# Kernel tuning notes

Hardware: AMD Instinct MI355X
Metric: run time of the kernel (lower is better)

Reference implementation:

```python
import jax, jax.numpy as jnp
import numpy as np

N = 100_000      # atom_count
E = 6_400_000    # number of (directed) edges, avg degree 64
BOX = 100.0      # simulation box edge length


def setup_inputs() -> dict:
    key = jax.random.key(0)
    k1, k2, k3 = jax.random.split(key, 3)
    pos = jax.random.uniform(k1, (N, 3), dtype=jnp.float32) * BOX
    src = jax.random.randint(k2, (E,), 0, N, dtype=jnp.int32)
    # offset in [1, N) guarantees dst != src (no zero-distance self edges)
    off = jax.random.randint(k3, (E,), 1, N, dtype=jnp.int32)
    dst = ((src + off) % N).astype(jnp.int32)
    edge_index = jnp.stack([src, dst], axis=0)  # [2, E]
    sigma = jnp.asarray(0.3, dtype=jnp.float32)
    epsilon = jnp.asarray(1.0, dtype=jnp.float32)
    return {"pos": pos, "sigma": sigma, "epsilon": epsilon, "edge_index": edge_index}


def _total_energy(pos, sigma, epsilon, src, dst):
    # r = edge_attr: per-edge distance, differentiable w.r.t. pos
    d = pos[src] - pos[dst]                      # [E, 3] gather + subtract
    r = jnp.sqrt(jnp.sum(d * d, axis=-1))        # [E]
    sr6 = (sigma / r) ** 6
    # potential_formula: 4*epsilon*((sigma/r)**12 - (sigma/r)**6)
    v_r = 4.0 * epsilon * (sr6 * sr6 - sr6)      # [E]
    return v_r.sum()


def reference(pos, sigma, epsilon, edge_index):
    src, dst = edge_index[0], edge_index[1]
    energy = _total_energy(pos, sigma, epsilon, src, dst)
    # afc: autograd force — grad of summed pair potential w.r.t. positions
    # (per-edge force scattered onto atoms by edge_index; grad does the
    #  gather-compute-scatter in one pass)
    pair_force = jax.grad(_total_energy, argnums=0)(pos, sigma, epsilon, src, dst)
    atom_force = -pair_force / 2.0               # /2: each pair counted twice
    return energy, atom_force
```

## Files before the change

kernel.cpp:

```cpp
#include <hip/hip_runtime.h>


#define NBINS      8
#define BIN_ATOMS  12800
#define BIN_F      (BIN_ATOMS * 3)
#define ROW_F      (NBINS * BIN_F)
#define BLOCK      1024
#define MAXCHUNKS  32

__global__ __launch_bounds__(BLOCK, 1) void pairforce_binned(
    const float* __restrict__ pos,
    const float* __restrict__ sigma_p,
    const float* __restrict__ eps_p,
    const int*   __restrict__ src,
    const int*   __restrict__ dst,
    float* __restrict__ frep,
    float* __restrict__ erep,
    int nEdges, int chunkEdges)
{
    extern __shared__ float sh[];
    const int t = threadIdx.x;
    const int b = blockIdx.x % NBINS;
    const int c = blockIdx.x / NBINS;

    for (int j = t; j < (BIN_F + 16) / 4; j += BLOCK)
        ((float4*)sh)[j] = make_float4(0.f, 0.f, 0.f, 0.f);
    __syncthreads();

    const float sigma = sigma_p[0];
    const float eps   = eps_p[0];
    const float sig2  = sigma * sigma;
    const int binStart = b * BIN_ATOMS;

    const int start = c * chunkEdges;
    const int end   = min(start + chunkEdges, nEdges);

    const int4* src4 = (const int4*)src;
    const int4* dst4 = (const int4*)dst;

    float ev = 0.0f;

    for (int i4 = (start >> 2) + t; i4 < (end >> 2); i4 += BLOCK) {
        const int4 s4 = src4[i4];
        const int4 d4 = dst4[i4];
        #pragma unroll
        for (int k = 0; k < 4; ++k) {
            const int s = (k == 0) ? s4.x : (k == 1) ? s4.y : (k == 2) ? s4.z : s4.w;
            const int d = (k == 0) ? d4.x : (k == 1) ? d4.y : (k == 2) ? d4.z : d4.w;
            const unsigned ls = (unsigned)(s - binStart);
            const unsigned ld = (unsigned)(d - binStart);
            const bool hs = ls < BIN_ATOMS;
            const bool hd = ld < BIN_ATOMS;
            if (hs | hd) {
                const float dx = pos[3 * s + 0] - pos[3 * d + 0];
                const float dy = pos[3 * s + 1] - pos[3 * d + 1];
                const float dz = pos[3 * s + 2] - pos[3 * d + 2];
                const float r2     = dx * dx + dy * dy + dz * dz;
                const float inv_r2 = 1.0f / r2;
                const float s2     = sig2 * inv_r2;
                const float sr6    = s2 * s2 * s2;
                const float sr12   = sr6 * sr6;
                const float fs = 12.0f * eps * (2.0f * sr12 - sr6) * inv_r2;
                const float fx = fs * dx;
                const float fy = fs * dy;
                const float fz = fs * dz;
                if (hs) {
                    atomicAdd(&sh[3 * ls + 0],  fx);
                    atomicAdd(&sh[3 * ls + 1],  fy);
                    atomicAdd(&sh[3 * ls + 2],  fz);
                    ev += 4.0f * eps * (sr12 - sr6);
                }
                if (hd) {
                    atomicAdd(&sh[3 * ld + 0], -fx);
                    atomicAdd(&sh[3 * ld + 1], -fy);
                    atomicAdd(&sh[3 * ld + 2], -fz);
                }
            }
        }
    }

    #pragma unroll
    for (int off = 32; off > 0; off >>= 1)
        ev += __shfl_down(ev, off, 64);
    if ((t & 63) == 0) sh[BIN_F + (t >> 6)] = ev;
    __syncthreads();

    float4* outSeg = (float4*)(frep + (size_t)c * ROW_F + (size_t)b * BIN_F);
    for (int j = t; j < BIN_F / 4; j += BLOCK)
        outSeg[j] = ((float4*)sh)[j];

    if (t == 0) {
        float e = 0.f;
        #pragma unroll
        for (int w = 0; w < 16; ++w) e += sh[BIN_F + w];
        erep[blockIdx.x] = e;
    }
}

__global__ __launch_bounds__(256) void pairforce_reduce(
    const float* __restrict__ frep,
    const float* __restrict__ erep,
    float* __restrict__ out,
    int n3, int nChunks, int nPart)
{
    const int i = blockIdx.x * 256 + threadIdx.x;
    if (i < n3) {
        float acc = 0.f;
        for (int c = 0; c < nChunks; ++c)
            acc += frep[(size_t)c * ROW_F + i];
        out[1 + i] = acc;
    }
    if (blockIdx.x == gridDim.x - 1) {
        float e = 0.f;
        for (int j = threadIdx.x; j < nPart; j += 256) e += erep[j];
        #pragma unroll
        for (int off = 32; off > 0; off >>= 1) e += __shfl_down(e, off, 64);
        __shared__ float ep[4];
        if ((threadIdx.x & 63) == 0) ep[threadIdx.x >> 6] = e;
        __syncthreads();
        if (threadIdx.x == 0) out[0] = ep[0] + ep[1] + ep[2] + ep[3];
    }
}

extern "C" void kernel_launch(void* const* d_in, const int* in_sizes, int n_in,
                              void* d_out, int out_size, void* d_ws, size_t ws_size,
                              hipStream_t stream)
{
    const float* pos     = (const float*)d_in[0];
    const float* sigma_p = (const float*)d_in[1];
    const float* eps_p   = (const float*)d_in[2];
    const int*   edge    = (const int*)d_in[3];

    const int nEdges = in_sizes[3] / 2;
    const int* src = edge;
    const int* dst = edge + nEdges;

    const int n3 = out_size - 1;

    const size_t rowBytes = (size_t)ROW_F * sizeof(float);
    int nChunks = (int)((ws_size - 4096) / rowBytes);
    if (nChunks > MAXCHUNKS) nChunks = MAXCHUNKS;
    if (nChunks < 1) nChunks = 1;

    const int chunkEdges = (((nEdges + nChunks - 1) / nChunks) + 3) & ~3;

    float* frep = (float*)d_ws;
    float* erep = frep + (size_t)nChunks * ROW_F;

    const size_t shbytes = (size_t)(BIN_F + 16) * sizeof(float);

    const int grid1 = nChunks * NBINS;
    pairforce_binned<<<grid1, BLOCK, shbytes, stream>>>(
        pos, sigma_p, eps_p, src, dst, frep, erep, nEdges, chunkEdges);

    const int grid2 = (n3 + 255) / 256;
    pairforce_reduce<<<grid2, 256, 0, stream>>>(
        frep, erep, (float*)d_out, n3, nChunks, nChunks * NBINS);
}
```

Before: 313.1 us.

## Pre-bucket edges by atom bin before shared-memory force accumulation

Adds a scatter pass that writes each directed edge as two compact records into per-wave, per-bin buckets, and pads positions to float4. The accumulation kernel then processes only the records for its bin, with positions staged in LDS. This replaces the old scheme in which every bin block rescanned the full edge list, cutting redundant global index reads. The trade-off is extra bucket write and read traffic, fixed bucket capacities that could silently drop edges if a bin overflows, and dependence on the atom count fitting the bin layout.

```diff
diff --git a/kernel.cpp b/kernel.cpp
--- a/kernel.cpp
+++ b/kernel.cpp
@@ -1,12 +1,177 @@
 #include <hip/hip_runtime.h>
 
+
+#define ROW_F   307200
+
+#define NB2     16
+#define BA2     6400
+#define BF2     (BA2 * 3)
+#define KCH     16
+#define SCG     256
+#define SCB     512
+#define NWAVES  2048
+#define CAP     512
 
 #define NBINS      8
 #define BIN_ATOMS  12800
 #define BIN_F      (BIN_ATOMS * 3)
-#define ROW_F      (NBINS * BIN_F)
 #define BLOCK      1024
 #define MAXCHUNKS  32
+
+__global__ __launch_bounds__(SCB) void pf_scatter(
+    const float* __restrict__ pos,
+    float4*      __restrict__ pos4,
+    const int*   __restrict__ src,
+    const int*   __restrict__ dst,
+    unsigned*    __restrict__ buckets,
+    unsigned*    __restrict__ cnt,
+    int nEdges, int nAtoms)
+{
+    __shared__ unsigned shcur[(SCB / 64) * NB2];
+    const int t = threadIdx.x, lane = t & 63, wv = t >> 6;
+    if (t < (SCB / 64) * NB2) shcur[t] = 0;
+
+    for (int i = blockIdx.x * SCB + t; i < nAtoms; i += SCG * SCB)
+        pos4[i] = make_float4(pos[3 * i + 0], pos[3 * i + 1], pos[3 * i + 2], 0.f);
+
+    __syncthreads();
+
+    unsigned* mycur = shcur + wv * NB2;
+    const int w    = blockIdx.x * (SCB / 64) + wv;
+    const int epw  = (nEdges + NWAVES - 1) / NWAVES;
+    const int ebeg = w * epw;
+    const int eend = min(nEdges, ebeg + epw);
+
+    int  e   = ebeg + lane;
+    bool act = e < eend;
+    int  s = 0, d = 0;
+    if (act) { s = src[e]; d = dst[e]; }
+
+    for (int base = ebeg; base < eend; base += 64) {
+        const int  en   = base + 64 + lane;
+        const bool actn = en < eend;
+        int sn = 0, dn = 0;
+        if (actn) { sn = src[en]; dn = dst[en]; }
+        if (act) {
+            const unsigned su = (unsigned)s, du = (unsigned)d;
+            const unsigned sb = su / BA2, db = du / BA2;
+            const unsigned recS = ((su - sb * BA2) << 18) | (1u << 17) | du;
+            const unsigned recD = ((du - db * BA2) << 18) | su;
+            const unsigned is = atomicAdd(&mycur[sb], 1u);
+            if (is < CAP) buckets[((size_t)w * NB2 + sb) * CAP + is] = recS;
+            const unsigned id = atomicAdd(&mycur[db], 1u);
+            if (id < CAP) buckets[((size_t)w * NB2 + db) * CAP + id] = recD;
+        }
+        act = actn; s = sn; d = dn;
+    }
+    __syncthreads();
+    if (lane < NB2) {
+        const unsigned cv = mycur[lane];
+        cnt[w * NB2 + lane] = cv < CAP ? cv : CAP;
+    }
+}
+
+__global__ __launch_bounds__(1024, 1) void pf_accum(
+    const float*    __restrict__ pos,
+    const float4*   __restrict__ pos4,
+    const float*    __restrict__ sigma_p,
+    const float*    __restrict__ eps_p,
+    const unsigned* __restrict__ buckets,
+    const unsigned* __restrict__ cnt,
+    float* __restrict__ frep,
+    float* __restrict__ erep,
+    int nAtoms)
+{
+    extern __shared__ float sh[];
+    float* shp = sh + BF2 + 16;
+    const int t = threadIdx.x, lane = t & 63, v = t >> 6;
+    const int b = blockIdx.x / KCH;
+    const int c = blockIdx.x % KCH;
+
+    for (int j = t; j < (BF2 + 16) / 4; j += 1024)
+        ((float4*)sh)[j] = make_float4(0.f, 0.f, 0.f, 0.f);
+
+    const int binStart = b * BA2;
+    const int binCnt   = min(BA2, nAtoms - binStart);
+    const int nf       = binCnt * 3;
+    const float4* gp   = (const float4*)(pos + (size_t)binStart * 3);
+    for (int j = t; j < (nf >> 2); j += 1024) ((float4*)shp)[j] = gp[j];
+    for (int j = (nf & ~3) + t; j < nf; j += 1024) shp[j] = pos[binStart * 3 + j];
+    __syncthreads();
+
+    const float sigma = sigma_p[0], eps = eps_p[0];
+    const float sig2 = sigma * sigma;
+    const float c12 = 12.f * eps, c4 = 4.f * eps;
+
+    float ev = 0.f;
+    const int slot = c * 16 + v;
+    for (int k = 0; k < NWAVES / 256; ++k) {
+        const int w = slot + (k << 8);
+        const int n = cnt[w * NB2 + b];
+        const unsigned* seg = buckets + ((size_t)w * NB2 + b) * CAP;
+        for (int j = lane; j < n; j += 64) {
+            const unsigned rec = seg[j];
+            const int   la = rec >> 18;
+            const int   o  = rec & 0x1FFFF;
+            const float fl = (rec & (1u << 17)) ? 1.f : 0.f;
+            const float ax = shp[3 * la + 0];
+            const float ay = shp[3 * la + 1];
+            const float az = shp[3 * la + 2];
+            const float4 po = pos4[o];
+            const float dx = ax - po.x, dy = ay - po.y, dz = az - po.z;
+            const float r2   = dx * dx + dy * dy + dz * dz;
+            const float ir2  = 1.0f / r2;
+            const float s2   = sig2 * ir2;
+            const float sr6  = s2 * s2 * s2;
+            const float sr12 = sr6 * sr6;
+            const float fs   = c12 * (2.f * sr12 - sr6) * ir2;
+            atomicAdd(&sh[3 * la + 0], fs * dx);
+            atomicAdd(&sh[3 * la + 1], fs * dy);
+            atomicAdd(&sh[3 * la + 2], fs * dz);
+            ev += fl * c4 * (sr12 - sr6);
+        }
+    }
+
+    #pragma unroll
+    for (int off = 32; off > 0; off >>= 1) ev += __shfl_down(ev, off, 64);
+    if (lane == 0) sh[BF2 + v] = ev;
+    __syncthreads();
+
+    float4* outSeg = (float4*)(frep + (size_t)c * ROW_F + (size_t)b * BF2);
+    for (int j = t; j < BF2 / 4; j += 1024) outSeg[j] = ((float4*)sh)[j];
+
+    if (t == 0) {
+        float e = 0.f;
+        #pragma unroll
+        for (int w2 = 0; w2 < 16; ++w2) e += sh[BF2 + w2];
+        erep[blockIdx.x] = e;
+    }
+}
+
+__global__ __launch_bounds__(256) void pairforce_reduce(
+    const float* __restrict__ frep,
+    const float* __restrict__ erep,
+    float* __restrict__ out,
+    int n3, int nChunks, int nPart)
+{
+    const int i = blockIdx.x * 256 + threadIdx.x;
+    if (i < n3) {
+        float acc = 0.f;
+        for (int c = 0; c < nChunks; ++c)
+            acc += frep[(size_t)c * ROW_F + i];
+        out[1 + i] = acc;
+    }
+    if (blockIdx.x == gridDim.x - 1) {
+        float e = 0.f;
+        for (int j = threadIdx.x; j < nPart; j += 256) e += erep[j];
+        #pragma unroll
+        for (int off = 32; off > 0; off >>= 1) e += __shfl_down(e, off, 64);
+        __shared__ float ep[4];
+        if ((threadIdx.x & 63) == 0) ep[threadIdx.x >> 6] = e;
+        __syncthreads();
+        if (threadIdx.x == 0) out[0] = ep[0] + ep[1] + ep[2] + ep[3];
+    }
+}
 
 __global__ __launch_bounds__(BLOCK, 1) void pairforce_binned(
     const float* __restrict__ pos,
@@ -97,31 +262,6 @@
     }
 }
 
-__global__ __launch_bounds__(256) void pairforce_reduce(
-    const float* __restrict__ frep,
-    const float* __restrict__ erep,
-    float* __restrict__ out,
-    int n3, int nChunks, int nPart)
-{
-    const int i = blockIdx.x * 256 + threadIdx.x;
-    if (i < n3) {
-        float acc = 0.f;
-        for (int c = 0; c < nChunks; ++c)
-            acc += frep[(size_t)c * ROW_F + i];
-        out[1 + i] = acc;
-    }
-    if (blockIdx.x == gridDim.x - 1) {
-        float e = 0.f;
-        for (int j = threadIdx.x; j < nPart; j += 256) e += erep[j];
-        #pragma unroll
-        for (int off = 32; off > 0; off >>= 1) e += __shfl_down(e, off, 64);
-        __shared__ float ep[4];
-        if ((threadIdx.x & 63) == 0) ep[threadIdx.x >> 6] = e;
-        __syncthreads();
-        if (threadIdx.x == 0) out[0] = ep[0] + ep[1] + ep[2] + ep[3];
-    }
-}
-
 extern "C" void kernel_launch(void* const* d_in, const int* in_sizes, int n_in,
                               void* d_out, int out_size, void* d_ws, size_t ws_size,
                               hipStream_t stream)
@@ -136,6 +276,26 @@
     const int* dst = edge + nEdges;
 
     const int n3 = out_size - 1;
+    const int nAtoms = n3 / 3;
+
+    size_t off = 0;
+    float*    pos4    = (float*)d_ws;                    off += (size_t)(NB2 * BA2) * 16;
+    unsigned* buckets = (unsigned*)((char*)d_ws + off);  off += (size_t)NWAVES * NB2 * CAP * 4;
+    unsigned* cntp    = (unsigned*)((char*)d_ws + off);  off += (size_t)NWAVES * NB2 * 4;
+    float*    frepN   = (float*)((char*)d_ws + off);     off += (size_t)KCH * ROW_F * 4;
+    float*    erepN   = (float*)((char*)d_ws + off);     off += 256 * 4;
+
+    if (ws_size >= off && nAtoms <= NB2 * BA2) {
+        pf_scatter<<<SCG, SCB, 0, stream>>>(pos, (float4*)pos4, src, dst,
+                                            buckets, cntp, nEdges, nAtoms);
+        const size_t shb = (size_t)(BF2 + 16 + BF2) * sizeof(float);
+        pf_accum<<<NB2 * KCH, 1024, shb, stream>>>(pos, (const float4*)pos4,
+                                                   sigma_p, eps_p, buckets, cntp,
+                                                   frepN, erepN, nAtoms);
+        pairforce_reduce<<<(n3 + 255) / 256, 256, 0, stream>>>(
+            frepN, erepN, (float*)d_out, n3, KCH, NB2 * KCH);
+        return;
+    }
 
     const size_t rowBytes = (size_t)ROW_F * sizeof(float);
     int nChunks = (int)((ws_size - 4096) / rowBytes);
```

Result: slower. 373.2 us (+19.2%).

## Bucket edges into atom-bin pair tiles and compute each edge once

Applied to the files above, without the earlier changes.

Adds a counting-sort pipeline: edges are counted and placed into per-tile buckets indexed by (min bin, max bin) pair across 32 atom bins. Each tile block then stages both bins' positions in LDS and computes each edge exactly once, accumulating forces for both endpoints in LDS. This replaces the old scheme, where each of 8 bins rescanned every edge and gathered positions from global memory. The cost is three extra preprocessing kernels that read the edge list twice and write a packed record array, plus per-tile load imbalance.

```diff
diff --git a/kernel.cpp b/kernel.cpp
--- a/kernel.cpp
+++ b/kernel.cpp
@@ -1,12 +1,252 @@
 #include <hip/hip_runtime.h>
 
+
+#define NBIN   32
+#define BA     3200
+#define BF     (BA * 3)
+#define NT     528
+#define SEGS   512
+#define ROW_F  307200
 
 #define NBINS      8
 #define BIN_ATOMS  12800
 #define BIN_F      (BIN_ATOMS * 3)
-#define ROW_F      (NBINS * BIN_F)
 #define BLOCK      1024
 #define MAXCHUNKS  32
+
+typedef __attribute__((ext_vector_type(4))) int ivec4;
+
+__device__ __forceinline__ ivec4 nt_load_i4(const int* p) {
+    return __builtin_nontemporal_load((const ivec4*)p);
+}
+__device__ __forceinline__ void lds_fadd(float* p, float v) {
+    __hip_atomic_fetch_add(p, v, __ATOMIC_RELAXED, __HIP_MEMORY_SCOPE_WORKGROUP);
+}
+__device__ __forceinline__ unsigned lds_uinc(unsigned* p) {
+    return __hip_atomic_fetch_add(p, 1u, __ATOMIC_RELAXED, __HIP_MEMORY_SCOPE_WORKGROUP);
+}
+
+__device__ __forceinline__ unsigned tile_of(unsigned bs, unsigned bd) {
+    const unsigned i = min(bs, bd), j = max(bs, bd);
+    return ((i * (2u * NBIN + 1u - i)) >> 1) + (j - i);
+}
+
+__global__ __launch_bounds__(1024) void pf_count(
+    const int* __restrict__ src, const int* __restrict__ dst,
+    unsigned* __restrict__ cnt, int nEdges)
+{
+    __shared__ unsigned c[NT];
+    const int t = threadIdx.x;
+    const int bid = (int)blockIdx.x;
+    if (t < NT) c[t] = 0;
+    __syncthreads();
+
+    const int eblk  = ((nEdges + SEGS - 1) / SEGS + 3) & ~3;
+    const int ebeg  = bid * eblk;
+    const int eend  = (ebeg + eblk < nEdges) ? (ebeg + eblk) : nEdges;
+    const int i4beg = ebeg >> 2;
+    const int i4end = eend >> 2;
+
+    for (int i4 = i4beg + t; i4 < i4end; i4 += 1024) {
+        const ivec4 s4 = nt_load_i4(src + 4 * i4);
+        const ivec4 d4 = nt_load_i4(dst + 4 * i4);
+        #pragma unroll
+        for (int k = 0; k < 4; ++k) {
+            const unsigned bs = (unsigned)s4[k] / BA;
+            const unsigned bd = (unsigned)d4[k] / BA;
+            lds_uinc(&c[tile_of(bs, bd)]);
+        }
+    }
+    __syncthreads();
+    if (t < NT) cnt[bid * NT + t] = c[t];
+}
+
+__global__ __launch_bounds__(1024) void pf_prefix(
+    const unsigned* __restrict__ cnt, unsigned* __restrict__ base,
+    unsigned* __restrict__ tileStart)
+{
+    __shared__ unsigned colTot[NT], ts[NT + 1];
+    const int t = threadIdx.x;
+    if (t < NT) {
+        unsigned run = 0;
+        for (int s = 0; s < SEGS; ++s) {
+            base[s * NT + t] = run;
+            run += cnt[s * NT + t];
+        }
+        colTot[t] = run;
+    }
+    __syncthreads();
+    if (t == 0) {
+        unsigned run = 0;
+        for (int k = 0; k < NT; ++k) { ts[k] = run; run += colTot[k]; }
+        ts[NT] = run;
+    }
+    __syncthreads();
+    if (t < NT) {
+        const unsigned add = ts[t];
+        for (int s = 0; s < SEGS; ++s) base[s * NT + t] += add;
+    }
+    if (t <= NT) tileStart[t] = ts[t];
+}
+
+__global__ __launch_bounds__(1024) void pf_place(
+    const int* __restrict__ src, const int* __restrict__ dst,
+    const unsigned* __restrict__ base, unsigned* __restrict__ recs, int nEdges)
+{
+    __shared__ unsigned cur[NT];
+    const int t = threadIdx.x;
+    const int bid = (int)blockIdx.x;
+    if (t < NT) cur[t] = base[bid * NT + t];
+    __syncthreads();
+
+    const int eblk  = ((nEdges + SEGS - 1) / SEGS + 3) & ~3;
+    const int ebeg  = bid * eblk;
+    const int eend  = (ebeg + eblk < nEdges) ? (ebeg + eblk) : nEdges;
+    const int i4beg = ebeg >> 2;
+    const int i4end = eend >> 2;
+
+    for (int i4 = i4beg + t; i4 < i4end; i4 += 1024) {
+        const ivec4 s4 = nt_load_i4(src + 4 * i4);
+        const ivec4 d4 = nt_load_i4(dst + 4 * i4);
+        #pragma unroll
+        for (int k = 0; k < 4; ++k) {
+            const unsigned su = (unsigned)s4[k], du = (unsigned)d4[k];
+            const unsigned bs = su / BA, bd = du / BA;
+            unsigned a = su, b = du;
+            if (bd < bs) { a = du; b = su; }
+            const unsigned i = min(bs, bd), j = max(bs, bd);
+            const unsigned li = a - i * BA, lj = b - j * BA;
+            const unsigned tl = ((i * (2u * NBIN + 1u - i)) >> 1) + (j - i);
+            const unsigned idx = lds_uinc(&cur[tl]);
+            recs[idx] = (li << 12) | lj;
+        }
+    }
+}
+
+__global__ __launch_bounds__(1024) void pf_accum2(
+    const float* __restrict__ pos,
+    const float* __restrict__ sigma_p, const float* __restrict__ eps_p,
+    const unsigned* __restrict__ recs, const unsigned* __restrict__ tileStart,
+    float* __restrict__ frep,
+    float* __restrict__ erep,
+    int nAtoms)
+{
+    extern __shared__ float sh[];
+    const int t = threadIdx.x, lane = t & 63, v = t >> 6;
+
+    int i = 0, rem = (int)blockIdx.x;
+    while (rem >= NBIN - i) { rem -= NBIN - i; ++i; }
+    const int j = i + rem;
+    const bool diag = (i == j);
+
+    float* sPosI = sh;
+    float* sPosJ = diag ? sh : sh + BF;
+    float* sFI   = sh + 2 * BF;
+    float* sFJ   = diag ? sFI : sh + 3 * BF;
+    float* sE    = sh + 4 * BF;
+
+    for (int k = t; k < (2 * BF + 16) / 4; k += 1024)
+        ((float4*)(sh + 2 * BF))[k] = make_float4(0.f, 0.f, 0.f, 0.f);
+
+    {
+        const int aI = i * BA;
+        int nf = nAtoms - aI; if (nf > BA) nf = BA; if (nf < 0) nf = 0; nf *= 3;
+        const float* g = pos + (size_t)aI * 3;
+        for (int k = t; k < (nf >> 2); k += 1024) ((float4*)sPosI)[k] = ((const float4*)g)[k];
+        for (int k = (nf & ~3) + t; k < nf; k += 1024) sPosI[k] = g[k];
+    }
+    if (!diag) {
+        const int aJ = j * BA;
+        int nf = nAtoms - aJ; if (nf > BA) nf = BA; if (nf < 0) nf = 0; nf *= 3;
+        const float* g = pos + (size_t)aJ * 3;
+        for (int k = t; k < (nf >> 2); k += 1024) ((float4*)sPosJ)[k] = ((const float4*)g)[k];
+        for (int k = (nf & ~3) + t; k < nf; k += 1024) sPosJ[k] = g[k];
+    }
+    __syncthreads();
+
+    const float sigma = sigma_p[0], eps = eps_p[0];
+    const float sig2 = sigma * sigma;
+    const float c12 = 12.f * eps, c4 = 4.f * eps;
+
+    const int rBeg = (int)tileStart[blockIdx.x];
+    const int rEnd = (int)tileStart[blockIdx.x + 1];
+    float ev = 0.f;
+
+    for (int r0 = rBeg; r0 < rEnd; r0 += 4 * 1024) {
+        unsigned rc[4]; bool ac[4];
+        #pragma unroll
+        for (int k = 0; k < 4; ++k) {
+            const int idx = r0 + k * 1024 + t;
+            ac[k] = idx < rEnd;
+            rc[k] = ac[k] ? recs[idx] : 0u;
+        }
+        #pragma unroll
+        for (int k = 0; k < 4; ++k) {
+            const int li = rc[k] >> 12, lj = rc[k] & 0xFFF;
+            const float ax = sPosI[3 * li + 0], ay = sPosI[3 * li + 1], az = sPosI[3 * li + 2];
+            const float bx = sPosJ[3 * lj + 0], by = sPosJ[3 * lj + 1], bz = sPosJ[3 * lj + 2];
+            const float dx = ax - bx, dy = ay - by, dz = az - bz;
+            const float r2   = dx * dx + dy * dy + dz * dz;
+            const float ir2  = 1.0f / r2;
+            const float s2   = sig2 * ir2;
+            const float sr6  = s2 * s2 * s2;
+            const float sr12 = sr6 * sr6;
+            const float fs   = c12 * (2.f * sr12 - sr6) * ir2;
+            if (ac[k]) {
+                lds_fadd(&sFI[3 * li + 0],  fs * dx);
+                lds_fadd(&sFI[3 * li + 1],  fs * dy);
+                lds_fadd(&sFI[3 * li + 2],  fs * dz);
+                lds_fadd(&sFJ[3 * lj + 0], -fs * dx);
+                lds_fadd(&sFJ[3 * lj + 1], -fs * dy);
+                lds_fadd(&sFJ[3 * lj + 2], -fs * dz);
+                ev += c4 * (sr12 - sr6);
+            }
+        }
+    }
+
+    #pragma unroll
+    for (int off = 32; off > 0; off >>= 1) ev += __shfl_down(ev, off, 64);
+    if (lane == 0) sE[v] = ev;
+    __syncthreads();
+
+    float4* dI = (float4*)(frep + (size_t)j * ROW_F + (size_t)i * BF);
+    for (int k = t; k < BF / 4; k += 1024) dI[k] = ((float4*)sFI)[k];
+    if (!diag) {
+        float4* dJ = (float4*)(frep + (size_t)i * ROW_F + (size_t)j * BF);
+        for (int k = t; k < BF / 4; k += 1024) dJ[k] = ((float4*)sFJ)[k];
+    }
+    if (t == 0) {
+        float e = 0.f;
+        #pragma unroll
+        for (int w = 0; w < 16; ++w) e += sE[w];
+        erep[blockIdx.x] = e;
+    }
+}
+
+__global__ __launch_bounds__(256) void pairforce_reduce(
+    const float* __restrict__ frep,
+    const float* __restrict__ erep,
+    float* __restrict__ out,
+    int n3, int nChunks, int nPart)
+{
+    const int i = blockIdx.x * 256 + threadIdx.x;
+    if (i < n3) {
+        float acc = 0.f;
+        for (int c = 0; c < nChunks; ++c)
+            acc += frep[(size_t)c * ROW_F + i];
+        out[1 + i] = acc;
+    }
+    if (blockIdx.x == gridDim.x - 1) {
+        float e = 0.f;
+        for (int jj = threadIdx.x; jj < nPart; jj += 256) e += erep[jj];
+        #pragma unroll
+        for (int off = 32; off > 0; off >>= 1) e += __shfl_down(e, off, 64);
+        __shared__ float ep[4];
+        if ((threadIdx.x & 63) == 0) ep[threadIdx.x >> 6] = e;
+        __syncthreads();
+        if (threadIdx.x == 0) out[0] = ep[0] + ep[1] + ep[2] + ep[3];
+    }
+}
 
 __global__ __launch_bounds__(BLOCK, 1) void pairforce_binned(
     const float* __restrict__ pos,
@@ -23,8 +263,8 @@
     const int b = blockIdx.x % NBINS;
     const int c = blockIdx.x / NBINS;
 
-    for (int j = t; j < (BIN_F + 16) / 4; j += BLOCK)
-        ((float4*)sh)[j] = make_float4(0.f, 0.f, 0.f, 0.f);
+    for (int jj = t; jj < (BIN_F + 16) / 4; jj += BLOCK)
+        ((float4*)sh)[jj] = make_float4(0.f, 0.f, 0.f, 0.f);
     __syncthreads();
 
     const float sigma = sigma_p[0];
@@ -86,39 +326,14 @@
     __syncthreads();
 
     float4* outSeg = (float4*)(frep + (size_t)c * ROW_F + (size_t)b * BIN_F);
-    for (int j = t; j < BIN_F / 4; j += BLOCK)
-        outSeg[j] = ((float4*)sh)[j];
+    for (int jj = t; jj < BIN_F / 4; jj += BLOCK)
+        outSeg[jj] = ((float4*)sh)[jj];
 
     if (t == 0) {
         float e = 0.f;
         #pragma unroll
         for (int w = 0; w < 16; ++w) e += sh[BIN_F + w];
         erep[blockIdx.x] = e;
-    }
-}
-
-__global__ __launch_bounds__(256) void pairforce_reduce(
-    const float* __restrict__ frep,
-    const float* __restrict__ erep,
-    float* __restrict__ out,
-    int n3, int nChunks, int nPart)
-{
-    const int i = blockIdx.x * 256 + threadIdx.x;
-    if (i < n3) {
-        float acc = 0.f;
-        for (int c = 0; c < nChunks; ++c)
-            acc += frep[(size_t)c * ROW_F + i];
-        out[1 + i] = acc;
-    }
-    if (blockIdx.x == gridDim.x - 1) {
-        float e = 0.f;
-        for (int j = threadIdx.x; j < nPart; j += 256) e += erep[j];
-        #pragma unroll
-        for (int off = 32; off > 0; off >>= 1) e += __shfl_down(e, off, 64);
-        __shared__ float ep[4];
-        if ((threadIdx.x & 63) == 0) ep[threadIdx.x >> 6] = e;
-        __syncthreads();
-        if (threadIdx.x == 0) out[0] = ep[0] + ep[1] + ep[2] + ep[3];
     }
 }
 
@@ -136,6 +351,28 @@
     const int* dst = edge + nEdges;
 
     const int n3 = out_size - 1;
+    const int nAtoms = n3 / 3;
+
+    auto alignup = [](size_t x) { return (x + 255) & ~(size_t)255; };
+    size_t off = 0;
+    unsigned* recs   = (unsigned*)((char*)d_ws + off); off = alignup(off + (size_t)nEdges * 4);
+    unsigned* cntp   = (unsigned*)((char*)d_ws + off); off = alignup(off + (size_t)SEGS * NT * 4);
+    unsigned* basep  = (unsigned*)((char*)d_ws + off); off = alignup(off + (size_t)SEGS * NT * 4);
+    unsigned* tstart = (unsigned*)((char*)d_ws + off); off = alignup(off + (size_t)(NT + 1) * 4);
+    float*    frepN  = (float*)((char*)d_ws + off);    off = alignup(off + (size_t)NBIN * ROW_F * 4);
+    float*    erepN  = (float*)((char*)d_ws + off);    off = alignup(off + (size_t)NT * 4);
+
+    if (ws_size >= off && nAtoms <= NBIN * BA && nEdges > 0 && (nEdges & 3) == 0) {
+        pf_count<<<SEGS, 1024, 0, stream>>>(src, dst, cntp, nEdges);
+        pf_prefix<<<1, 1024, 0, stream>>>(cntp, basep, tstart);
+        pf_place<<<SEGS, 1024, 0, stream>>>(src, dst, basep, recs, nEdges);
+        const size_t shb = (size_t)(4 * BF + 16) * sizeof(float);
+        pf_accum2<<<NT, 1024, shb, stream>>>(pos, sigma_p, eps_p, recs, tstart,
+                                             frepN, erepN, nAtoms);
+        pairforce_reduce<<<(n3 + 255) / 256, 256, 0, stream>>>(
+            frepN, erepN, (float*)d_out, n3, NBIN, NT);
+        return;
+    }
 
     const size_t rowBytes = (size_t)ROW_F * sizeof(float);
     int nChunks = (int)((ws_size - 4096) / rowBytes);
```

Result: slower. 559.1 us (+78.6%).

## Bucket edges by atom bin via counting sort before force accumulation

Applied to the files above, without the earlier changes.

Replaces the chunk×bin scan, in which every block reads all edges of its chunk, with a counting-sort pipeline. Edges are histogrammed into segment/bin/column buckets, prefix-scanned, and written out as packed per-endpoint records. The accumulate kernel then reads only the records for its own bin and keeps that bin's positions in LDS. This removes the redundant edge reads across bins, at the cost of several extra kernel launches and a full pass writing and reading 2E records. It falls back to the old path when the workspace or input shape does not fit.

```diff
diff --git a/kernel.cpp b/kernel.cpp
--- a/kernel.cpp
+++ b/kernel.cpp
@@ -1,12 +1,267 @@
 #include <hip/hip_runtime.h>
 
+
+#define NBIN   32
+#define BA     3200
+#define BF     (BA * 3)
+#define SEGS   256
+#define NCOL   64
+#define BPS    (NBIN * NCOL)
+#define NBUCK  (SEGS * BPS)
+#define NROW   16
+#define ROW_F  307200
 
 #define NBINS      8
 #define BIN_ATOMS  12800
 #define BIN_F      (BIN_ATOMS * 3)
-#define ROW_F      (NBINS * BIN_F)
 #define BLOCK      1024
 #define MAXCHUNKS  32
+
+typedef __attribute__((ext_vector_type(4))) int ivec4;
+
+__device__ __forceinline__ ivec4 nt_load_i4(const int* p) {
+    return __builtin_nontemporal_load((const ivec4*)p);
+}
+__device__ __forceinline__ void lds_fadd(float* p, float v) {
+    __hip_atomic_fetch_add(p, v, __ATOMIC_RELAXED, __HIP_MEMORY_SCOPE_WORKGROUP);
+}
+__device__ __forceinline__ unsigned lds_uinc(unsigned* p) {
+    return __hip_atomic_fetch_add(p, 1u, __ATOMIC_RELAXED, __HIP_MEMORY_SCOPE_WORKGROUP);
+}
+
+__global__ __launch_bounds__(1024) void pf_count(
+    const float* __restrict__ pos, float4* __restrict__ pos4,
+    const int* __restrict__ src, const int* __restrict__ dst,
+    unsigned* __restrict__ cnt, int nEdges, int nAtoms)
+{
+    __shared__ unsigned h[BPS];
+    const int t = threadIdx.x, bid = (int)blockIdx.x;
+    h[t] = 0; h[t + 1024] = 0;
+
+    for (int i = bid * 1024 + t; i < nAtoms; i += SEGS * 1024)
+        pos4[i] = make_float4(pos[3 * i + 0], pos[3 * i + 1], pos[3 * i + 2], 0.f);
+    __syncthreads();
+
+    const int eblk  = ((nEdges + SEGS - 1) / SEGS + 3) & ~3;
+    const int ebeg  = bid * eblk;
+    const int eend  = (ebeg + eblk < nEdges) ? (ebeg + eblk) : nEdges;
+    for (int i4 = (ebeg >> 2) + t; i4 < (eend >> 2); i4 += 1024) {
+        const ivec4 s4 = nt_load_i4(src + 4 * i4);
+        const ivec4 d4 = nt_load_i4(dst + 4 * i4);
+        #pragma unroll
+        for (int k = 0; k < 4; ++k) {
+            const unsigned su = (unsigned)s4[k], du = (unsigned)d4[k];
+            lds_uinc(&h[(su / BA) * NCOL + (su & 63u)]);
+            lds_uinc(&h[(du / BA) * NCOL + (du & 63u)]);
+        }
+    }
+    __syncthreads();
+    cnt[bid * BPS + t] = h[t];
+    cnt[bid * BPS + 1024 + t] = h[t + 1024];
+}
+
+__global__ __launch_bounds__(1024) void pf_scanA(
+    const unsigned* __restrict__ cnt, unsigned* __restrict__ bstart,
+    unsigned* __restrict__ btot)
+{
+    __shared__ unsigned wt[16], wo[16];
+    const int t = threadIdx.x, lane = t & 63, wv = t >> 6;
+    const int gid = (int)blockIdx.x * 1024 + t;
+    const unsigned v = cnt[gid];
+    unsigned x = v;
+    #pragma unroll
+    for (int off = 1; off < 64; off <<= 1) {
+        const unsigned n = __shfl_up(x, off, 64);
+        if (lane >= off) x += n;
+    }
+    if (lane == 63) wt[wv] = x;
+    __syncthreads();
+    if (t == 0) {
+        unsigned run = 0;
+        #pragma unroll
+        for (int w = 0; w < 16; ++w) { wo[w] = run; run += wt[w]; }
+        btot[blockIdx.x] = run;
+    }
+    __syncthreads();
+    bstart[gid] = (x - v) + wo[wv];
+}
+
+__global__ __launch_bounds__(512) void pf_scanB(
+    const unsigned* __restrict__ btot, unsigned* __restrict__ boffs)
+{
+    __shared__ unsigned wt[8], wo[8];
+    const int t = threadIdx.x, lane = t & 63, wv = t >> 6;
+    const unsigned v = btot[t];
+    unsigned x = v;
+    #pragma unroll
+    for (int off = 1; off < 64; off <<= 1) {
+        const unsigned n = __shfl_up(x, off, 64);
+        if (lane >= off) x += n;
+    }
+    if (lane == 63) wt[wv] = x;
+    __syncthreads();
+    if (t == 0) {
+        unsigned run = 0;
+        #pragma unroll
+        for (int w = 0; w < 8; ++w) { wo[w] = run; run += wt[w]; }
+    }
+    __syncthreads();
+    boffs[t] = (x - v) + wo[wv];
+}
+
+__global__ __launch_bounds__(1024) void pf_scanC(
+    unsigned* __restrict__ bstart, const unsigned* __restrict__ boffs, int nRec)
+{
+    const int gid = (int)blockIdx.x * 1024 + threadIdx.x;
+    bstart[gid] += boffs[blockIdx.x];
+    if (gid == 0) bstart[NBUCK] = (unsigned)nRec;
+}
+
+__global__ __launch_bounds__(1024) void pf_place(
+    const int* __restrict__ src, const int* __restrict__ dst,
+    const unsigned* __restrict__ bstart, unsigned* __restrict__ recs, int nEdges)
+{
+    __shared__ unsigned cur[BPS];
+    const int t = threadIdx.x, bid = (int)blockIdx.x;
+    cur[t] = bstart[bid * BPS + t];
+    cur[t + 1024] = bstart[bid * BPS + 1024 + t];
+    __syncthreads();
+
+    const int eblk  = ((nEdges + SEGS - 1) / SEGS + 3) & ~3;
+    const int ebeg  = bid * eblk;
+    const int eend  = (ebeg + eblk < nEdges) ? (ebeg + eblk) : nEdges;
+    for (int i4 = (ebeg >> 2) + t; i4 < (eend >> 2); i4 += 1024) {
+        const ivec4 s4 = nt_load_i4(src + 4 * i4);
+        const ivec4 d4 = nt_load_i4(dst + 4 * i4);
+        #pragma unroll
+        for (int k = 0; k < 4; ++k) {
+            const unsigned su = (unsigned)s4[k], du = (unsigned)d4[k];
+            const unsigned ob_s = su / BA, ob_d = du / BA;
+            const unsigned is = lds_uinc(&cur[ob_s * NCOL + (su & 63u)]);
+            recs[is] = ((su - ob_s * BA) << 18) | (1u << 17) | du;
+            const unsigned id = lds_uinc(&cur[ob_d * NCOL + (du & 63u)]);
+            recs[id] = ((du - ob_d * BA) << 18) | su;
+        }
+    }
+}
+
+__global__ __launch_bounds__(512) void pf_accum3(
+    const float* __restrict__ pos, const float4* __restrict__ pos4,
+    const float* __restrict__ sigma_p, const float* __restrict__ eps_p,
+    const unsigned* __restrict__ recs, const unsigned* __restrict__ bstart,
+    float* __restrict__ frep,
+    float* __restrict__ erep,
+    int nAtoms)
+{
+    extern __shared__ float sh[];
+    float* sF = sh;
+    float* sE = sh + BF;
+    float* sP = sh + BF + 8;
+    const int t = threadIdx.x, lane = t & 63, wv = t >> 6;
+    const int obin = (int)blockIdx.x >> 4;
+    const int SC   = (int)blockIdx.x & 15;
+
+    for (int k = t; k < (BF + 8) / 4; k += 512)
+        ((float4*)sF)[k] = make_float4(0.f, 0.f, 0.f, 0.f);
+    {
+        const int aS = obin * BA;
+        int nf = nAtoms - aS; if (nf > BA) nf = BA; if (nf < 0) nf = 0; nf *= 3;
+        const float* g = pos + (size_t)aS * 3;
+        for (int k = t; k < (nf >> 2); k += 512) ((float4*)sP)[k] = ((const float4*)g)[k];
+        for (int k = (nf & ~3) + t; k < nf; k += 512) sP[k] = g[k];
+    }
+    __syncthreads();
+
+    const float sigma = sigma_p[0], eps = eps_p[0];
+    const float sig2 = sigma * sigma;
+    const float c12 = 12.f * eps, c4 = 4.f * eps;
+
+    float ev = 0.f;
+    #pragma unroll
+    for (int q = 0; q < 2; ++q) {
+        const int seg = SC * 16 + (t >> 6) + q * 8;
+        const int bkt = seg * BPS + obin * NCOL + (t & 63);
+        const int beg = (int)bstart[bkt];
+        const int end = (int)bstart[bkt + 1];
+
+        for (int r = beg; r < end; r += 2) {
+            const unsigned rec0 = recs[r];
+            const bool v1 = (r + 1) < end;
+            const unsigned rec1 = v1 ? recs[r + 1] : 0u;
+            const int l0 = rec0 >> 18, o0 = rec0 & 0x1FFFF;
+            const int l1 = rec1 >> 18, o1 = rec1 & 0x1FFFF;
+            const float4 p0 = pos4[o0];
+            const float4 p1 = pos4[o1];
+            const float a0x = sP[3 * l0 + 0], a0y = sP[3 * l0 + 1], a0z = sP[3 * l0 + 2];
+            const float a1x = sP[3 * l1 + 0], a1y = sP[3 * l1 + 1], a1z = sP[3 * l1 + 2];
+
+            const float d0x = a0x - p0.x, d0y = a0y - p0.y, d0z = a0z - p0.z;
+            const float r20  = d0x * d0x + d0y * d0y + d0z * d0z;
+            const float ir20 = 1.0f / r20;
+            const float s20  = sig2 * ir20;
+            const float sr60 = s20 * s20 * s20;
+            const float sr120 = sr60 * sr60;
+            const float fs0  = c12 * (2.f * sr120 - sr60) * ir20;
+
+            const float d1x = a1x - p1.x, d1y = a1y - p1.y, d1z = a1z - p1.z;
+            const float r21  = d1x * d1x + d1y * d1y + d1z * d1z;
+            const float ir21 = 1.0f / r21;
+            const float s21  = sig2 * ir21;
+            const float sr61 = s21 * s21 * s21;
+            const float sr121 = sr61 * sr61;
+            const float fs1  = c12 * (2.f * sr121 - sr61) * ir21;
+
+            lds_fadd(&sF[3 * l0 + 0], fs0 * d0x);
+            lds_fadd(&sF[3 * l0 + 1], fs0 * d0y);
+            lds_fadd(&sF[3 * l0 + 2], fs0 * d0z);
+            ev += (rec0 & (1u << 17)) ? c4 * (sr120 - sr60) : 0.f;
+            if (v1) {
+                lds_fadd(&sF[3 * l1 + 0], fs1 * d1x);
+                lds_fadd(&sF[3 * l1 + 1], fs1 * d1y);
+                lds_fadd(&sF[3 * l1 + 2], fs1 * d1z);
+                ev += (rec1 & (1u << 17)) ? c4 * (sr121 - sr61) : 0.f;
+            }
+        }
+    }
+
+    #pragma unroll
+    for (int off = 32; off > 0; off >>= 1) ev += __shfl_down(ev, off, 64);
+    if (lane == 0) sE[wv] = ev;
+    __syncthreads();
+
+    float4* d = (float4*)(frep + (size_t)SC * ROW_F + (size_t)obin * BF);
+    for (int k = t; k < BF / 4; k += 512) d[k] = ((const float4*)sF)[k];
+    if (t == 0) {
+        float e = 0.f;
+        #pragma unroll
+        for (int w = 0; w < 8; ++w) e += sE[w];
+        erep[blockIdx.x] = e;
+    }
+}
+
+__global__ __launch_bounds__(256) void pairforce_reduce(
+    const float* __restrict__ frep,
+    const float* __restrict__ erep,
+    float* __restrict__ out, int n3, int nChunks, int nPart)
+{
+    const int i = blockIdx.x * 256 + threadIdx.x;
+    if (i < n3) {
+        float acc = 0.f;
+        for (int c = 0; c < nChunks; ++c)
+            acc += frep[(size_t)c * ROW_F + i];
+        out[1 + i] = acc;
+    }
+    if (blockIdx.x == gridDim.x - 1) {
+        float e = 0.f;
+        for (int jj = threadIdx.x; jj < nPart; jj += 256) e += erep[jj];
+        #pragma unroll
+        for (int off = 32; off > 0; off >>= 1) e += __shfl_down(e, off, 64);
+        __shared__ float ep[4];
+        if ((threadIdx.x & 63) == 0) ep[threadIdx.x >> 6] = e;
+        __syncthreads();
+        if (threadIdx.x == 0) out[0] = ep[0] + ep[1] + ep[2] + ep[3];
+    }
+}
 
 __global__ __launch_bounds__(BLOCK, 1) void pairforce_binned(
     const float* __restrict__ pos,
@@ -23,8 +278,8 @@
     const int b = blockIdx.x % NBINS;
     const int c = blockIdx.x / NBINS;
 
-    for (int j = t; j < (BIN_F + 16) / 4; j += BLOCK)
-        ((float4*)sh)[j] = make_float4(0.f, 0.f, 0.f, 0.f);
+    for (int jj = t; jj < (BIN_F + 16) / 4; jj += BLOCK)
+        ((float4*)sh)[jj] = make_float4(0.f, 0.f, 0.f, 0.f);
     __syncthreads();
 
     const float sigma = sigma_p[0];
@@ -86,39 +341,14 @@
     __syncthreads();
 
     float4* outSeg = (float4*)(frep + (size_t)c * ROW_F + (size_t)b * BIN_F);
-    for (int j = t; j < BIN_F / 4; j += BLOCK)
-        outSeg[j] = ((float4*)sh)[j];
+    for (int jj = t; jj < BIN_F / 4; jj += BLOCK)
+        outSeg[jj] = ((float4*)sh)[jj];
 
     if (t == 0) {
         float e = 0.f;
         #pragma unroll
         for (int w = 0; w < 16; ++w) e += sh[BIN_F + w];
         erep[blockIdx.x] = e;
-    }
-}
-
-__global__ __launch_bounds__(256) void pairforce_reduce(
-    const float* __restrict__ frep,
-    const float* __restrict__ erep,
-    float* __restrict__ out,
-    int n3, int nChunks, int nPart)
-{
-    const int i = blockIdx.x * 256 + threadIdx.x;
-    if (i < n3) {
-        float acc = 0.f;
-        for (int c = 0; c < nChunks; ++c)
-            acc += frep[(size_t)c * ROW_F + i];
-        out[1 + i] = acc;
-    }
-    if (blockIdx.x == gridDim.x - 1) {
-        float e = 0.f;
-        for (int j = threadIdx.x; j < nPart; j += 256) e += erep[j];
-        #pragma unroll
-        for (int off = 32; off > 0; off >>= 1) e += __shfl_down(e, off, 64);
-        __shared__ float ep[4];
-        if ((threadIdx.x & 63) == 0) ep[threadIdx.x >> 6] = e;
-        __syncthreads();
-        if (threadIdx.x == 0) out[0] = ep[0] + ep[1] + ep[2] + ep[3];
     }
 }
 
@@ -136,6 +366,35 @@
     const int* dst = edge + nEdges;
 
     const int n3 = out_size - 1;
+    const int nAtoms = n3 / 3;
+    const int nRec = 2 * nEdges;
+
+    auto alignup = [](size_t x) { return (x + 255) & ~(size_t)255; };
+    size_t off = 0;
+    unsigned* recs   = (unsigned*)((char*)d_ws + off); off = alignup(off + (size_t)nRec * 4);
+    unsigned* cntp   = (unsigned*)((char*)d_ws + off); off = alignup(off + (size_t)NBUCK * 4);
+    unsigned* bstart = (unsigned*)((char*)d_ws + off); off = alignup(off + (size_t)(NBUCK + 1) * 4);
+    unsigned* btot   = (unsigned*)((char*)d_ws + off); off = alignup(off + 512 * 4);
+    unsigned* boffs  = (unsigned*)((char*)d_ws + off); off = alignup(off + 512 * 4);
+    float*    pos4   = (float*)((char*)d_ws + off);    off = alignup(off + (size_t)(NBIN * BA) * 16);
+    float*    frepN  = (float*)((char*)d_ws + off);    off = alignup(off + (size_t)NROW * ROW_F * 4);
+    float*    erepN  = (float*)((char*)d_ws + off);    off = alignup(off + (size_t)(NBIN * NROW) * 4);
+
+    if (ws_size >= off && nAtoms <= NBIN * BA && nEdges > 0 && (nEdges & 3) == 0) {
+        pf_count<<<SEGS, 1024, 0, stream>>>(pos, (float4*)pos4, src, dst,
+                                            cntp, nEdges, nAtoms);
+        pf_scanA<<<NBUCK / 1024, 1024, 0, stream>>>(cntp, bstart, btot);
+        pf_scanB<<<1, 512, 0, stream>>>(btot, boffs);
+        pf_scanC<<<NBUCK / 1024, 1024, 0, stream>>>(bstart, boffs, nRec);
+        pf_place<<<SEGS, 1024, 0, stream>>>(src, dst, bstart, recs, nEdges);
+        const size_t shb = (size_t)(2 * BF + 8) * sizeof(float);
+        pf_accum3<<<NBIN * NROW, 512, shb, stream>>>(pos, (const float4*)pos4,
+                                                     sigma_p, eps_p, recs, bstart,
+                                                     frepN, erepN, nAtoms);
+        pairforce_reduce<<<(n3 + 255) / 256, 256, 0, stream>>>(
+            frepN, erepN, (float*)d_out, n3, NROW, NBIN * NROW);
+        return;
+    }
 
     const size_t rowBytes = (size_t)ROW_F * sizeof(float);
     int nChunks = (int)((ws_size - 4096) / rowBytes);
```

New measurement: 514.4 us. 1.64x slower.
